# Performance work log

Measured on AMD Instinct MI355X. Metric: run time of the kernel, lower is better.

The kernel has to match this reference:

```python
import jax, jax.numpy as jnp
import numpy as np

N = 50000
E = 600000
H = 128
LN_EPS = 1e-5


def _layer_norm(h, g, b):
    mu = jnp.mean(h, axis=-1, keepdims=True)
    var = jnp.var(h, axis=-1, keepdims=True)
    return (h - mu) * jax.lax.rsqrt(var + LN_EPS) * g + b


def _mlp(h, params):
    # params = (w0, b0, w1, b1, w2, b2, ln_g, ln_b); mlp_layers=2 pattern:
    # Linear->ReLU->Linear->ReLU->Linear->LayerNorm
    w0, b0, w1, b1, w2, b2, g, be = params
    h = jax.nn.relu(h @ w0 + b0)
    h = jax.nn.relu(h @ w1 + b1)
    h = h @ w2 + b2
    return _layer_norm(h, g, be)


def setup_inputs() -> dict:
    key = jax.random.key(0)
    ks = jax.random.split(key, 16)
    def lin(k, fan_in, fan_out):
        lim = 1.0 / np.sqrt(fan_in)
        kw, kb = jax.random.split(k)
        w = jax.random.uniform(kw, (fan_in, fan_out), jnp.float32, -lim, lim)
        b = jax.random.uniform(kb, (fan_out,), jnp.float32, -lim, lim)
        return w, b
    x = jax.random.normal(ks[0], (N, H), jnp.float32)
    e = jax.random.normal(ks[1], (E, H), jnp.float32)
    edge_index = jax.random.randint(ks[2], (2, E), 0, N, jnp.int64)
    we0, be0 = lin(ks[3], 3 * H, H)
    we1, be1 = lin(ks[4], H, H)
    we2, be2 = lin(ks[5], H, H)
    wn0, bn0 = lin(ks[6], 2 * H, H)
    wn1, bn1 = lin(ks[7], H, H)
    wn2, bn2 = lin(ks[8], H, H)
    return {
        "x": x, "e": e, "edge_index": edge_index,
        "we0": we0, "be0": be0, "we1": we1, "be1": be1, "we2": we2, "be2": be2,
        "ge": jnp.ones((H,), jnp.float32), "bge": jnp.zeros((H,), jnp.float32),
        "wn0": wn0, "bn0": bn0, "wn1": wn1, "bn1": bn1, "wn2": wn2, "bn2": bn2,
        "gn": jnp.ones((H,), jnp.float32), "bgn": jnp.zeros((H,), jnp.float32),
    }


def reference(x, e, edge_index,
              we0, be0, we1, be1, we2, be2, ge, bge,
              wn0, bn0, wn1, bn1, wn2, bn2, gn, bgn):
    src = edge_index[0]
    dst = edge_index[1]
    # gather node feats per edge -> [E, 3H] -> edge MLP -> [E, H]
    edge_in = jnp.concatenate([x[dst], x[src], e], axis=-1)
    e_new = _mlp(edge_in, (we0, be0, we1, be1, we2, be2, ge, bge))
    # scatter-add edge messages into destination nodes -> [N, H]
    agg = jax.ops.segment_sum(e_new, dst, num_segments=x.shape[0])
    node_in = jnp.concatenate([x, agg], axis=-1)
    x_new = x + _mlp(node_in, (wn0, bn0, wn1, bn1, wn2, bn2, gn, bgn))
    return (x_new, e_new)
```

## Files before the change

### kernel.cpp

```cpp
#include <hip/hip_runtime.h>

#define NN 50000
#define NE 600000
#define HD 128

typedef __attribute__((ext_vector_type(8))) short short8;
typedef __attribute__((ext_vector_type(4))) float floatx4;

__device__ __forceinline__ unsigned short f2bf(float f) {
  unsigned int u = __builtin_bit_cast(unsigned int, f);
  u += 0x7FFFu + ((u >> 16) & 1u);
  return (unsigned short)(u >> 16);
}

__global__ void pack_w(const float* __restrict__ w, unsigned short* __restrict__ wp,
                       int total) {
  int p = blockIdx.x * blockDim.x + threadIdx.x;
  if (p >= total) return;
  int j = p & 7, lane = (p >> 3) & 63, t = p >> 9;
  int n0 = t & 7, k0 = t >> 3;
  int k = k0 * 32 + (lane >> 4) * 8 + j;
  int n = n0 * 16 + (lane & 15);
  wp[p] = f2bf(w[k * HD + n]);
}

template <int KSTEPS>
__device__ __forceinline__ void gemm_tile(const unsigned short* a_base, int a_stride,
                                          const unsigned short* __restrict__ wp,
                                          int lane, floatx4* acc) {
  int quad = lane >> 4, l16 = lane & 15;
  for (int k0 = 0; k0 < KSTEPS; ++k0) {
    short8 a = *(const short8*)(a_base + l16 * a_stride + k0 * 32 + quad * 8);
    const unsigned short* w = wp + k0 * 4096 + lane * 8;
#pragma unroll
    for (int n0 = 0; n0 < 8; ++n0) {
      short8 b = *(const short8*)(w + n0 * 512);
      acc[n0] = __builtin_amdgcn_mfma_f32_16x16x32_bf16(a, b, acc[n0], 0, 0, 0);
    }
  }
}

__device__ __forceinline__ void store_relu_bf16(const floatx4* acc,
                                                const float* __restrict__ bias,
                                                unsigned short* out_base, int stride,
                                                int lane) {
  int quad = lane >> 4, l16 = lane & 15;
#pragma unroll
  for (int n0 = 0; n0 < 8; ++n0) {
    float bv = bias[n0 * 16 + l16];
#pragma unroll
    for (int r = 0; r < 4; ++r) {
      float v = acc[n0][r] + bv;
      v = v > 0.f ? v : 0.f;
      out_base[(quad * 4 + r) * stride + n0 * 16 + l16] = f2bf(v);
    }
  }
}

#define SIN 392
#define SH 136
#define SNI 264

__global__ __launch_bounds__(256) void edge_kernel(
    const float* __restrict__ x, const float* __restrict__ e,
    const int* __restrict__ idx, const unsigned short* __restrict__ w0p,
    const float* __restrict__ b0, const unsigned short* __restrict__ w1p,
    const float* __restrict__ b1, const unsigned short* __restrict__ w2p,
    const float* __restrict__ b2, const float* __restrict__ g,
    const float* __restrict__ bg, float* __restrict__ e_out,
    float* __restrict__ agg) {
  __shared__ __align__(16) unsigned short lin[64 * SIN];
  __shared__ __align__(16) unsigned short lh[64 * SH];
  __shared__ int sdst[64];

  int wave = threadIdx.x >> 6, lane = threadIdx.x & 63;
  int quad = lane >> 4, l16 = lane & 15;
  int ebase = blockIdx.x * 64;

  for (int r = wave * 16; r < wave * 16 + 16; ++r) {
    int ei = ebase + r;
    int s = idx[ei], d = idx[NE + ei];
    if (lane == 0) sdst[r] = d;
    const float* xd = x + (size_t)d * HD;
    const float* xs = x + (size_t)s * HD;
    const float* ee = e + (size_t)ei * HD;
    unsigned short* row = lin + r * SIN;
    row[lane] = f2bf(xd[lane]);
    row[64 + lane] = f2bf(xd[64 + lane]);
    row[128 + lane] = f2bf(xs[lane]);
    row[192 + lane] = f2bf(xs[64 + lane]);
    row[256 + lane] = f2bf(ee[lane]);
    row[320 + lane] = f2bf(ee[64 + lane]);
  }

  floatx4 acc[8];
  floatx4 z = {0.f, 0.f, 0.f, 0.f};

#pragma unroll
  for (int t = 0; t < 8; ++t) acc[t] = z;
  gemm_tile<12>(lin + wave * 16 * SIN, SIN, w0p, lane, acc);
  store_relu_bf16(acc, b0, lh + wave * 16 * SH, SH, lane);

  unsigned short* h2 = lin + wave * 16 * SIN;
#pragma unroll
  for (int t = 0; t < 8; ++t) acc[t] = z;
  gemm_tile<4>(lh + wave * 16 * SH, SH, w1p, lane, acc);
  store_relu_bf16(acc, b1, h2, SH, lane);

#pragma unroll
  for (int t = 0; t < 8; ++t) acc[t] = z;
  gemm_tile<4>(h2, SH, w2p, lane, acc);

  float h3[8][4];
#pragma unroll
  for (int n0 = 0; n0 < 8; ++n0) {
    float bv = b2[n0 * 16 + l16];
#pragma unroll
    for (int r = 0; r < 4; ++r) h3[n0][r] = acc[n0][r] + bv;
  }
  float s1[4] = {0.f, 0.f, 0.f, 0.f}, s2[4] = {0.f, 0.f, 0.f, 0.f};
#pragma unroll
  for (int n0 = 0; n0 < 8; ++n0)
#pragma unroll
    for (int r = 0; r < 4; ++r) {
      s1[r] += h3[n0][r];
      s2[r] += h3[n0][r] * h3[n0][r];
    }
#pragma unroll
  for (int m = 1; m < 16; m <<= 1) {
#pragma unroll
    for (int r = 0; r < 4; ++r) {
      s1[r] += __shfl_xor(s1[r], m, 64);
      s2[r] += __shfl_xor(s2[r], m, 64);
    }
  }
  float mu[4], rs[4];
#pragma unroll
  for (int r = 0; r < 4; ++r) {
    mu[r] = s1[r] * (1.f / 128.f);
    float var = s2[r] * (1.f / 128.f) - mu[r] * mu[r];
    rs[r] = rsqrtf(var + 1e-5f);
  }
#pragma unroll
  for (int n0 = 0; n0 < 8; ++n0) {
    int col = n0 * 16 + l16;
    float gv = g[col], bv = bg[col];
#pragma unroll
    for (int r = 0; r < 4; ++r) {
      int rl = wave * 16 + quad * 4 + r;
      int ei = ebase + rl;
      float v = (h3[n0][r] - mu[r]) * rs[r] * gv + bv;
      e_out[(size_t)ei * HD + col] = v;
      atomicAdd(&agg[(size_t)sdst[rl] * HD + col], v);
    }
  }
}

__global__ __launch_bounds__(256) void node_kernel(
    const float* __restrict__ x, const float* __restrict__ agg,
    const unsigned short* __restrict__ w0p, const float* __restrict__ b0,
    const unsigned short* __restrict__ w1p, const float* __restrict__ b1,
    const unsigned short* __restrict__ w2p, const float* __restrict__ b2,
    const float* __restrict__ g, const float* __restrict__ bg,
    float* __restrict__ x_out) {
  __shared__ __align__(16) unsigned short lin[64 * SNI];
  __shared__ __align__(16) unsigned short lh[64 * SH];

  int wave = threadIdx.x >> 6, lane = threadIdx.x & 63;
  int quad = lane >> 4, l16 = lane & 15;
  int nbase = blockIdx.x * 64;

  for (int r = wave * 16; r < wave * 16 + 16; ++r) {
    int ni = nbase + r;
    int nc = ni < NN ? ni : NN - 1;
    const float* xr = x + (size_t)nc * HD;
    const float* ar = agg + (size_t)nc * HD;
    unsigned short* row = lin + r * SNI;
    row[lane] = f2bf(xr[lane]);
    row[64 + lane] = f2bf(xr[64 + lane]);
    row[128 + lane] = f2bf(ar[lane]);
    row[192 + lane] = f2bf(ar[64 + lane]);
  }

  floatx4 acc[8];
  floatx4 z = {0.f, 0.f, 0.f, 0.f};

#pragma unroll
  for (int t = 0; t < 8; ++t) acc[t] = z;
  gemm_tile<8>(lin + wave * 16 * SNI, SNI, w0p, lane, acc);
  store_relu_bf16(acc, b0, lh + wave * 16 * SH, SH, lane);

  unsigned short* h2 = lin + wave * 16 * SNI;
#pragma unroll
  for (int t = 0; t < 8; ++t) acc[t] = z;
  gemm_tile<4>(lh + wave * 16 * SH, SH, w1p, lane, acc);
  store_relu_bf16(acc, b1, h2, SH, lane);

#pragma unroll
  for (int t = 0; t < 8; ++t) acc[t] = z;
  gemm_tile<4>(h2, SH, w2p, lane, acc);

  float h3[8][4];
#pragma unroll
  for (int n0 = 0; n0 < 8; ++n0) {
    float bv = b2[n0 * 16 + l16];
#pragma unroll
    for (int r = 0; r < 4; ++r) h3[n0][r] = acc[n0][r] + bv;
  }
  float s1[4] = {0.f, 0.f, 0.f, 0.f}, s2[4] = {0.f, 0.f, 0.f, 0.f};
#pragma unroll
  for (int n0 = 0; n0 < 8; ++n0)
#pragma unroll
    for (int r = 0; r < 4; ++r) {
      s1[r] += h3[n0][r];
      s2[r] += h3[n0][r] * h3[n0][r];
    }
#pragma unroll
  for (int m = 1; m < 16; m <<= 1) {
#pragma unroll
    for (int r = 0; r < 4; ++r) {
      s1[r] += __shfl_xor(s1[r], m, 64);
      s2[r] += __shfl_xor(s2[r], m, 64);
    }
  }
  float mu[4], rs[4];
#pragma unroll
  for (int r = 0; r < 4; ++r) {
    mu[r] = s1[r] * (1.f / 128.f);
    float var = s2[r] * (1.f / 128.f) - mu[r] * mu[r];
    rs[r] = rsqrtf(var + 1e-5f);
  }
#pragma unroll
  for (int n0 = 0; n0 < 8; ++n0) {
    int col = n0 * 16 + l16;
    float gv = g[col], bv = bg[col];
#pragma unroll
    for (int r = 0; r < 4; ++r) {
      int rl = wave * 16 + quad * 4 + r;
      int ni = nbase + rl;
      if (ni < NN) {
        float v = (h3[n0][r] - mu[r]) * rs[r] * gv + bv;
        x_out[(size_t)ni * HD + col] = x[(size_t)ni * HD + col] + v;
      }
    }
  }
}

extern "C" void kernel_launch(void* const* d_in, const int* in_sizes, int n_in,
                              void* d_out, int out_size, void* d_ws, size_t ws_size,
                              hipStream_t stream) {
  const float* x = (const float*)d_in[0];
  const float* e = (const float*)d_in[1];
  const int* idx = (const int*)d_in[2];
  const float* we0 = (const float*)d_in[3];
  const float* be0 = (const float*)d_in[4];
  const float* we1 = (const float*)d_in[5];
  const float* be1 = (const float*)d_in[6];
  const float* we2 = (const float*)d_in[7];
  const float* be2 = (const float*)d_in[8];
  const float* ge = (const float*)d_in[9];
  const float* bge = (const float*)d_in[10];
  const float* wn0 = (const float*)d_in[11];
  const float* bn0 = (const float*)d_in[12];
  const float* wn1 = (const float*)d_in[13];
  const float* bn1 = (const float*)d_in[14];
  const float* wn2 = (const float*)d_in[15];
  const float* bn2 = (const float*)d_in[16];
  const float* gn = (const float*)d_in[17];
  const float* bgn = (const float*)d_in[18];

  float* xout = (float*)d_out;
  float* eout = (float*)d_out + (size_t)NN * HD;

  unsigned short* ws = (unsigned short*)d_ws;
  unsigned short* w0p = ws;
  unsigned short* w1p = w0p + 384 * HD;
  unsigned short* w2p = w1p + HD * HD;
  unsigned short* wn0p = w2p + HD * HD;
  unsigned short* wn1p = wn0p + 256 * HD;
  unsigned short* wn2p = wn1p + HD * HD;

  hipMemsetAsync(xout, 0, (size_t)NN * HD * sizeof(float), stream);

  pack_w<<<(384 * HD + 255) / 256, 256, 0, stream>>>(we0, w0p, 384 * HD);
  pack_w<<<(HD * HD + 255) / 256, 256, 0, stream>>>(we1, w1p, HD * HD);
  pack_w<<<(HD * HD + 255) / 256, 256, 0, stream>>>(we2, w2p, HD * HD);
  pack_w<<<(256 * HD + 255) / 256, 256, 0, stream>>>(wn0, wn0p, 256 * HD);
  pack_w<<<(HD * HD + 255) / 256, 256, 0, stream>>>(wn1, wn1p, HD * HD);
  pack_w<<<(HD * HD + 255) / 256, 256, 0, stream>>>(wn2, wn2p, HD * HD);

  edge_kernel<<<NE / 64, 256, 0, stream>>>(x, e, idx, w0p, be0, w1p, be1, w2p, be2,
                                           ge, bge, eout, xout);
  node_kernel<<<(NN + 63) / 64, 256, 0, stream>>>(x, xout, wn0p, bn0, wn1p, bn1,
                                                  wn2p, bn2, gn, bgn, xout);
}
```

Baseline: 1.079 ms.

## Load MFMA A operands directly from global, pre-convert x to bf16, shrink LDS

Edge and node kernels no longer stage the gathered input rows in shared memory. Each lane loads its 8-element A fragment straight from global memory and converts it in registers. A bf16 copy of x is made once per call in workspace when space allows, which halves gather bytes for the x[src] and x[dst] rows. Shared memory drops to one hidden buffer reused across layers, and launch bounds request 4 blocks per CU for more occupancy. The trade-off is an extra conversion pass and scattered 16-byte global loads in place of coalesced row loads.

```diff
diff --git a/kernel.cpp b/kernel.cpp
--- a/kernel.cpp
+++ b/kernel.cpp
@@ -11,6 +11,17 @@
   unsigned int u = __builtin_bit_cast(unsigned int, f);
   u += 0x7FFFu + ((u >> 16) & 1u);
   return (unsigned short)(u >> 16);
+}
+
+__device__ __forceinline__ short8 cvt8(const float* __restrict__ p) {
+  floatx4 v0 = *(const floatx4*)p;
+  floatx4 v1 = *(const floatx4*)(p + 4);
+  short8 r;
+  r[0] = (short)f2bf(v0[0]); r[1] = (short)f2bf(v0[1]);
+  r[2] = (short)f2bf(v0[2]); r[3] = (short)f2bf(v0[3]);
+  r[4] = (short)f2bf(v1[0]); r[5] = (short)f2bf(v1[1]);
+  r[6] = (short)f2bf(v1[2]); r[7] = (short)f2bf(v1[3]);
+  return r;
 }
 
 __global__ void pack_w(const float* __restrict__ w, unsigned short* __restrict__ wp,
@@ -24,6 +35,14 @@
   wp[p] = f2bf(w[k * HD + n]);
 }
 
+__global__ void cvt_bf16(const float* __restrict__ in,
+                         unsigned short* __restrict__ out, int total8) {
+  int p = blockIdx.x * blockDim.x + threadIdx.x;
+  if (p >= total8) return;
+  short8 r = cvt8(in + (size_t)p * 8);
+  *(short8*)(out + (size_t)p * 8) = r;
+}
+
 template <int KSTEPS>
 __device__ __forceinline__ void gemm_tile(const unsigned short* a_base, int a_stride,
                                           const unsigned short* __restrict__ wp,
@@ -57,59 +76,81 @@
   }
 }
 
-#define SIN 392
 #define SH 136
-#define SNI 264
-
-__global__ __launch_bounds__(256) void edge_kernel(
-    const float* __restrict__ x, const float* __restrict__ e,
-    const int* __restrict__ idx, const unsigned short* __restrict__ w0p,
-    const float* __restrict__ b0, const unsigned short* __restrict__ w1p,
-    const float* __restrict__ b1, const unsigned short* __restrict__ w2p,
-    const float* __restrict__ b2, const float* __restrict__ g,
-    const float* __restrict__ bg, float* __restrict__ e_out,
-    float* __restrict__ agg) {
-  __shared__ __align__(16) unsigned short lin[64 * SIN];
+
+template <int XBF>
+__global__ __launch_bounds__(256, 4) void edge_kernel(
+    const float* __restrict__ x, const unsigned short* __restrict__ xb,
+    const float* __restrict__ e, const int* __restrict__ idx,
+    const unsigned short* __restrict__ w0p, const float* __restrict__ b0,
+    const unsigned short* __restrict__ w1p, const float* __restrict__ b1,
+    const unsigned short* __restrict__ w2p, const float* __restrict__ b2,
+    const float* __restrict__ g, const float* __restrict__ bg,
+    float* __restrict__ e_out, float* __restrict__ agg) {
   __shared__ __align__(16) unsigned short lh[64 * SH];
-  __shared__ int sdst[64];
 
   int wave = threadIdx.x >> 6, lane = threadIdx.x & 63;
   int quad = lane >> 4, l16 = lane & 15;
-  int ebase = blockIdx.x * 64;
-
-  for (int r = wave * 16; r < wave * 16 + 16; ++r) {
-    int ei = ebase + r;
-    int s = idx[ei], d = idx[NE + ei];
-    if (lane == 0) sdst[r] = d;
-    const float* xd = x + (size_t)d * HD;
-    const float* xs = x + (size_t)s * HD;
-    const float* ee = e + (size_t)ei * HD;
-    unsigned short* row = lin + r * SIN;
-    row[lane] = f2bf(xd[lane]);
-    row[64 + lane] = f2bf(xd[64 + lane]);
-    row[128 + lane] = f2bf(xs[lane]);
-    row[192 + lane] = f2bf(xs[64 + lane]);
-    row[256 + lane] = f2bf(ee[lane]);
-    row[320 + lane] = f2bf(ee[64 + lane]);
-  }
+  int ebase = blockIdx.x * 64 + wave * 16;
+  int arow = ebase + l16;
+  int s = idx[arow], d = idx[NE + arow];
 
   floatx4 acc[8];
   floatx4 z = {0.f, 0.f, 0.f, 0.f};
-
-#pragma unroll
-  for (int t = 0; t < 8; ++t) acc[t] = z;
-  gemm_tile<12>(lin + wave * 16 * SIN, SIN, w0p, lane, acc);
-  store_relu_bf16(acc, b0, lh + wave * 16 * SH, SH, lane);
-
-  unsigned short* h2 = lin + wave * 16 * SIN;
-#pragma unroll
-  for (int t = 0; t < 8; ++t) acc[t] = z;
-  gemm_tile<4>(lh + wave * 16 * SH, SH, w1p, lane, acc);
-  store_relu_bf16(acc, b1, h2, SH, lane);
-
-#pragma unroll
-  for (int t = 0; t < 8; ++t) acc[t] = z;
-  gemm_tile<4>(h2, SH, w2p, lane, acc);
+#pragma unroll
+  for (int t = 0; t < 8; ++t) acc[t] = z;
+
+  const float* ee = e + (size_t)arow * HD + quad * 8;
+  if constexpr (XBF) {
+    const unsigned short* xd = xb + (size_t)d * HD + quad * 8;
+    const unsigned short* xs = xb + (size_t)s * HD + quad * 8;
+#pragma unroll
+    for (int k0 = 0; k0 < 12; ++k0) {
+      short8 a;
+      if (k0 < 4)
+        a = *(const short8*)(xd + k0 * 32);
+      else if (k0 < 8)
+        a = *(const short8*)(xs + (k0 - 4) * 32);
+      else
+        a = cvt8(ee + (k0 - 8) * 32);
+      const unsigned short* w = w0p + k0 * 4096 + lane * 8;
+#pragma unroll
+      for (int n0 = 0; n0 < 8; ++n0) {
+        short8 b = *(const short8*)(w + n0 * 512);
+        acc[n0] = __builtin_amdgcn_mfma_f32_16x16x32_bf16(a, b, acc[n0], 0, 0, 0);
+      }
+    }
+  } else {
+    const float* xd = x + (size_t)d * HD + quad * 8;
+    const float* xs = x + (size_t)s * HD + quad * 8;
+#pragma unroll
+    for (int k0 = 0; k0 < 12; ++k0) {
+      short8 a;
+      if (k0 < 4)
+        a = cvt8(xd + k0 * 32);
+      else if (k0 < 8)
+        a = cvt8(xs + (k0 - 4) * 32);
+      else
+        a = cvt8(ee + (k0 - 8) * 32);
+      const unsigned short* w = w0p + k0 * 4096 + lane * 8;
+#pragma unroll
+      for (int n0 = 0; n0 < 8; ++n0) {
+        short8 b = *(const short8*)(w + n0 * 512);
+        acc[n0] = __builtin_amdgcn_mfma_f32_16x16x32_bf16(a, b, acc[n0], 0, 0, 0);
+      }
+    }
+  }
+  unsigned short* lhw = lh + wave * 16 * SH;
+  store_relu_bf16(acc, b0, lhw, SH, lane);
+
+#pragma unroll
+  for (int t = 0; t < 8; ++t) acc[t] = z;
+  gemm_tile<4>(lhw, SH, w1p, lane, acc);
+  store_relu_bf16(acc, b1, lhw, SH, lane);
+
+#pragma unroll
+  for (int t = 0; t < 8; ++t) acc[t] = z;
+  gemm_tile<4>(lhw, SH, w2p, lane, acc);
 
   float h3[8][4];
 #pragma unroll
@@ -141,64 +182,89 @@
     float var = s2[r] * (1.f / 128.f) - mu[r] * mu[r];
     rs[r] = rsqrtf(var + 1e-5f);
   }
+  int drow[4];
+#pragma unroll
+  for (int r = 0; r < 4; ++r) drow[r] = idx[NE + ebase + quad * 4 + r];
 #pragma unroll
   for (int n0 = 0; n0 < 8; ++n0) {
     int col = n0 * 16 + l16;
     float gv = g[col], bv = bg[col];
 #pragma unroll
     for (int r = 0; r < 4; ++r) {
-      int rl = wave * 16 + quad * 4 + r;
-      int ei = ebase + rl;
+      int ei = ebase + quad * 4 + r;
       float v = (h3[n0][r] - mu[r]) * rs[r] * gv + bv;
       e_out[(size_t)ei * HD + col] = v;
-      atomicAdd(&agg[(size_t)sdst[rl] * HD + col], v);
-    }
-  }
-}
-
-__global__ __launch_bounds__(256) void node_kernel(
-    const float* __restrict__ x, const float* __restrict__ agg,
-    const unsigned short* __restrict__ w0p, const float* __restrict__ b0,
-    const unsigned short* __restrict__ w1p, const float* __restrict__ b1,
-    const unsigned short* __restrict__ w2p, const float* __restrict__ b2,
-    const float* __restrict__ g, const float* __restrict__ bg,
-    float* __restrict__ x_out) {
-  __shared__ __align__(16) unsigned short lin[64 * SNI];
+      atomicAdd(&agg[(size_t)drow[r] * HD + col], v);
+    }
+  }
+}
+
+template <int XBF>
+__global__ __launch_bounds__(256, 4) void node_kernel(
+    const float* __restrict__ x, const unsigned short* __restrict__ xb,
+    const float* __restrict__ agg, const unsigned short* __restrict__ w0p,
+    const float* __restrict__ b0, const unsigned short* __restrict__ w1p,
+    const float* __restrict__ b1, const unsigned short* __restrict__ w2p,
+    const float* __restrict__ b2, const float* __restrict__ g,
+    const float* __restrict__ bg, float* __restrict__ x_out) {
   __shared__ __align__(16) unsigned short lh[64 * SH];
 
   int wave = threadIdx.x >> 6, lane = threadIdx.x & 63;
   int quad = lane >> 4, l16 = lane & 15;
-  int nbase = blockIdx.x * 64;
-
-  for (int r = wave * 16; r < wave * 16 + 16; ++r) {
-    int ni = nbase + r;
-    int nc = ni < NN ? ni : NN - 1;
-    const float* xr = x + (size_t)nc * HD;
-    const float* ar = agg + (size_t)nc * HD;
-    unsigned short* row = lin + r * SNI;
-    row[lane] = f2bf(xr[lane]);
-    row[64 + lane] = f2bf(xr[64 + lane]);
-    row[128 + lane] = f2bf(ar[lane]);
-    row[192 + lane] = f2bf(ar[64 + lane]);
-  }
+  int nbase = blockIdx.x * 64 + wave * 16;
+  int arow = nbase + l16;
+  int nc = arow < NN ? arow : NN - 1;
 
   floatx4 acc[8];
   floatx4 z = {0.f, 0.f, 0.f, 0.f};
-
-#pragma unroll
-  for (int t = 0; t < 8; ++t) acc[t] = z;
-  gemm_tile<8>(lin + wave * 16 * SNI, SNI, w0p, lane, acc);
-  store_relu_bf16(acc, b0, lh + wave * 16 * SH, SH, lane);
-
-  unsigned short* h2 = lin + wave * 16 * SNI;
-#pragma unroll
-  for (int t = 0; t < 8; ++t) acc[t] = z;
-  gemm_tile<4>(lh + wave * 16 * SH, SH, w1p, lane, acc);
-  store_relu_bf16(acc, b1, h2, SH, lane);
-
-#pragma unroll
-  for (int t = 0; t < 8; ++t) acc[t] = z;
-  gemm_tile<4>(h2, SH, w2p, lane, acc);
+#pragma unroll
+  for (int t = 0; t < 8; ++t) acc[t] = z;
+
+  const float* ar = agg + (size_t)nc * HD + quad * 8;
+  if constexpr (XBF) {
+    const unsigned short* xr = xb + (size_t)nc * HD + quad * 8;
+#pragma unroll
+    for (int k0 = 0; k0 < 8; ++k0) {
+      short8 a;
+      if (k0 < 4)
+        a = *(const short8*)(xr + k0 * 32);
+      else
+        a = cvt8(ar + (k0 - 4) * 32);
+      const unsigned short* w = w0p + k0 * 4096 + lane * 8;
+#pragma unroll
+      for (int n0 = 0; n0 < 8; ++n0) {
+        short8 b = *(const short8*)(w + n0 * 512);
+        acc[n0] = __builtin_amdgcn_mfma_f32_16x16x32_bf16(a, b, acc[n0], 0, 0, 0);
+      }
+    }
+  } else {
+    const float* xr = x + (size_t)nc * HD + quad * 8;
+#pragma unroll
+    for (int k0 = 0; k0 < 8; ++k0) {
+      short8 a;
+      if (k0 < 4)
+        a = cvt8(xr + k0 * 32);
+      else
+        a = cvt8(ar + (k0 - 4) * 32);
+      const unsigned short* w = w0p + k0 * 4096 + lane * 8;
+#pragma unroll
+      for (int n0 = 0; n0 < 8; ++n0) {
+        short8 b = *(const short8*)(w + n0 * 512);
+        acc[n0] = __builtin_amdgcn_mfma_f32_16x16x32_bf16(a, b, acc[n0], 0, 0, 0);
+      }
+    }
+  }
+  unsigned short* lhw = lh + wave * 16 * SH;
+  store_relu_bf16(acc, b0, lhw, SH, lane);
+
+#pragma unroll
+  for (int t = 0; t < 8; ++t) acc[t] = z;
+  gemm_tile<4>(lhw, SH, w1p, lane, acc);
+  store_relu_bf16(acc, b1, lhw, SH, lane);
+
+#pragma unroll
+  for (int t = 0; t < 8; ++t) acc[t] = z;
+  gemm_tile<4>(lhw, SH, w2p, lane, acc);
 
   float h3[8][4];
 #pragma unroll
@@ -236,8 +302,7 @@
     float gv = g[col], bv = bg[col];
 #pragma unroll
     for (int r = 0; r < 4; ++r) {
-      int rl = wave * 16 + quad * 4 + r;
-      int ni = nbase + rl;
+      int ni = nbase + quad * 4 + r;
       if (ni < NN) {
         float v = (h3[n0][r] - mu[r]) * rs[r] * gv + bv;
         x_out[(size_t)ni * HD + col] = x[(size_t)ni * HD + col] + v;
@@ -279,6 +344,10 @@
   unsigned short* wn0p = w2p + HD * HD;
   unsigned short* wn1p = wn0p + 256 * HD;
   unsigned short* wn2p = wn1p + HD * HD;
+  unsigned short* xb = wn2p + HD * HD;
+
+  size_t w_shorts = (size_t)(384 + 128 + 128 + 256 + 128 + 128) * HD;
+  bool use_xb = ws_size >= (w_shorts + (size_t)NN * HD) * sizeof(unsigned short);
 
   hipMemsetAsync(xout, 0, (size_t)NN * HD * sizeof(float), stream);
 
@@ -289,8 +358,16 @@
   pack_w<<<(HD * HD + 255) / 256, 256, 0, stream>>>(wn1, wn1p, HD * HD);
   pack_w<<<(HD * HD + 255) / 256, 256, 0, stream>>>(wn2, wn2p, HD * HD);
 
-  edge_kernel<<<NE / 64, 256, 0, stream>>>(x, e, idx, w0p, be0, w1p, be1, w2p, be2,
-                                           ge, bge, eout, xout);
-  node_kernel<<<(NN + 63) / 64, 256, 0, stream>>>(x, xout, wn0p, bn0, wn1p, bn1,
-                                                  wn2p, bn2, gn, bgn, xout);
-}
+  if (use_xb) {
+    cvt_bf16<<<(NN * HD / 8 + 255) / 256, 256, 0, stream>>>(x, xb, NN * HD / 8);
+    edge_kernel<1><<<NE / 64, 256, 0, stream>>>(x, xb, e, idx, w0p, be0, w1p, be1,
+                                                w2p, be2, ge, bge, eout, xout);
+    node_kernel<1><<<(NN + 63) / 64, 256, 0, stream>>>(
+        x, xb, xout, wn0p, bn0, wn1p, bn1, wn2p, bn2, gn, bgn, xout);
+  } else {
+    edge_kernel<0><<<NE / 64, 256, 0, stream>>>(x, xb, e, idx, w0p, be0, w1p, be1,
+                                                w2p, be2, ge, bge, eout, xout);
+    node_kernel<0><<<(NN + 63) / 64, 256, 0, stream>>>(
+        x, xb, xout, wn0p, bn0, wn1p, bn1, wn2p, bn2, gn, bgn, xout);
+  }
+}
```

New measurement: 990.6 us. -8.2%, faster.
